# Performance work log

Measured on AMD Instinct MI355X. Metric: run time of the kernel, lower is better.

The kernel has to match this reference:

```python
import jax, jax.numpy as jnp
import numpy as np

EMB = 256
N_NODES = 20000
N_EDGES = 200000


def _sage_layer(x, src, dst, edge_attr, W, b, n_nodes):
    # message = x[src] + edge_attr ; mean-aggregate into dst ; ReLU(Linear([x;agg]))
    msg = x[src] + edge_attr                                   # [2E, emb]
    s = jax.ops.segment_sum(msg, dst, num_segments=n_nodes)    # [N, emb]
    cnt = jax.ops.segment_sum(jnp.ones((dst.shape[0], 1), x.dtype), dst,
                              num_segments=n_nodes)            # [N, 1]
    agg = s / jnp.maximum(cnt, 1.0)
    return jax.nn.relu(jnp.concatenate([x, agg], axis=1) @ W + b)


def setup_inputs() -> dict:
    key = jax.random.key(0)
    ks = jax.random.split(key, 12)
    sc = 0.05
    inp = {
        "x": jax.random.normal(ks[0], (N_NODES, EMB), jnp.float32),
        "edge_attr": jax.random.normal(ks[1], (N_EDGES, EMB), jnp.float32),
        "batch_q_embds": jax.random.normal(ks[2], (N_EDGES, EMB), jnp.float32),
        "edge_index": jax.random.randint(ks[3], (2, N_EDGES), 0, N_NODES, jnp.int64
                                         if jax.config.jax_enable_x64 else jnp.int32),
        "W_rev1": jax.random.normal(ks[4], (EMB, EMB), jnp.float32) * sc,
        "b_rev1": jnp.zeros((EMB,), jnp.float32),
        "W_rev2": jax.random.normal(ks[5], (EMB, EMB), jnp.float32) * sc,
        "b_rev2": jnp.zeros((EMB,), jnp.float32),
        "W_sage1": jax.random.normal(ks[6], (2 * EMB, EMB), jnp.float32) * sc,
        "b_sage1": jnp.zeros((EMB,), jnp.float32),
        "W_sage2": jax.random.normal(ks[7], (2 * EMB, EMB), jnp.float32) * sc,
        "b_sage2": jnp.zeros((EMB,), jnp.float32),
        "W_pred1": jax.random.normal(ks[8], (6 * EMB, EMB), jnp.float32) * sc,
        "b_pred1": jnp.zeros((EMB,), jnp.float32),
        "W_pred2": jax.random.normal(ks[9], (EMB, 1), jnp.float32) * sc,
        "b_pred2": jnp.zeros((1,), jnp.float32),
    }
    return inp


def reference(x, edge_attr, batch_q_embds, edge_index,
              W_rev1, b_rev1, W_rev2, b_rev2,
              W_sage1, b_sage1, W_sage2, b_sage2,
              W_pred1, b_pred1, W_pred2, b_pred2):
    src, dst = edge_index[0], edge_index[1]
    # reverse-edge attributes via proj_reverse MLP
    edge_attr_rev = jax.nn.relu(edge_attr @ W_rev1 + b_rev1) @ W_rev2 + b_rev2
    src_f = jnp.concatenate([src, dst])          # [2E]
    dst_f = jnp.concatenate([dst, src])          # [2E]
    ea_f = jnp.concatenate([edge_attr, edge_attr_rev], axis=0)  # [2E, emb]
    # 2-layer GraphSAGE backbone over nodes, collect per-layer outputs
    h1 = _sage_layer(x, src_f, dst_f, ea_f, W_sage1, b_sage1, N_NODES)
    h2 = _sage_layer(h1, src_f, dst_f, ea_f, W_sage2, b_sage2, N_NODES)
    h_e = jnp.concatenate([h1, h2], axis=1)      # [N, 2*emb]
    # per-edge triple features: [q ; h_e[head] ; edge_attr ; h_e[tail]]
    h_triple = jnp.concatenate([batch_q_embds, h_e[src], edge_attr, h_e[dst]], axis=1)
    attn_logits = (jax.nn.relu(h_triple @ W_pred1 + b_pred1) @ W_pred2 + b_pred2)[:, 0]
    # idp-bern sampling (training=True): gumbel-like logistic noise, temp=1
    u = jax.random.uniform(jax.random.key(42), attn_logits.shape,
                           attn_logits.dtype, 1e-10, 1.0 - 1e-10)
    noise = jnp.log(u) - jnp.log(1.0 - u)
    sampled = jax.nn.sigmoid(attn_logits + noise)
    return attn_logits, sampled
```

## Files before the change

kernel.cpp:

```cpp
#include <hip/hip_runtime.h>
#include <cstdint>
#include <cstddef>

#define EMB 256
#define NN 20000
#define NE 200000
#define NE2 400000

typedef unsigned short ushort_t;
typedef __attribute__((ext_vector_type(8))) short bf16x8;
typedef __attribute__((ext_vector_type(4))) float f32x4;

__device__ __forceinline__ ushort_t f2bf(float f) {
    unsigned u = __float_as_uint(f);
    u += 0x7FFFu + ((u >> 16) & 1u);
    return (ushort_t)(u >> 16);
}
__device__ __forceinline__ float bf2f(ushort_t u) {
    return __uint_as_float(((unsigned)u) << 16);
}

__device__ __forceinline__ void async_cp16(const ushort_t* g, ushort_t* l) {
    __builtin_amdgcn_global_load_lds(
        (const __attribute__((address_space(1))) unsigned int*)g,
        (__attribute__((address_space(3))) unsigned int*)l,
        16, 0, 0);
}

__device__ __forceinline__ unsigned rotl32(unsigned v, int d) {
    return (v << d) | (v >> (32 - d));
}
__device__ __forceinline__ void threefry2x32(unsigned k0, unsigned k1,
                                             unsigned x0, unsigned x1,
                                             unsigned& o0, unsigned& o1) {
    unsigned k2 = k0 ^ k1 ^ 0x1BD11BDAu;
    x0 += k0; x1 += k1;
#define TF_R(r) { x0 += x1; x1 = rotl32(x1, (r)); x1 ^= x0; }
    TF_R(13) TF_R(15) TF_R(26) TF_R(6)
    x0 += k1; x1 += k2 + 1u;
    TF_R(17) TF_R(29) TF_R(16) TF_R(24)
    x0 += k2; x1 += k0 + 2u;
    TF_R(13) TF_R(15) TF_R(26) TF_R(6)
    x0 += k0; x1 += k1 + 3u;
    TF_R(17) TF_R(29) TF_R(16) TF_R(24)
    x0 += k1; x1 += k2 + 4u;
    TF_R(13) TF_R(15) TF_R(26) TF_R(6)
    x0 += k2; x1 += k0 + 5u;
#undef TF_R
    o0 = x0; o1 = x1;
}

__global__ void deg_kernel(const int* __restrict__ src, const int* __restrict__ dst,
                           int* __restrict__ deg) {
    int i = blockIdx.x * blockDim.x + threadIdx.x;
    if (i < NE2) {
        int n = (i < NE) ? dst[i] : src[i - NE];
        atomicAdd(&deg[n], 1);
    }
}

__global__ void prefix_kernel(const int* __restrict__ deg, int* __restrict__ row_start,
                              int* __restrict__ cursor) {
    __shared__ int sums[1024];
    int t = threadIdx.x;
    const int CH = (NN + 1023) / 1024;
    int lo = t * CH, hi = lo + CH;
    if (hi > NN) hi = NN;
    if (lo > NN) lo = NN;
    int s = 0;
    for (int n = lo; n < hi; n++) s += deg[n];
    sums[t] = s;
    __syncthreads();
    for (int off = 1; off < 1024; off <<= 1) {
        int v = (t >= off) ? sums[t - off] : 0;
        __syncthreads();
        sums[t] += v;
        __syncthreads();
    }
    int run = (t == 0) ? 0 : sums[t - 1];
    for (int n = lo; n < hi; n++) {
        row_start[n] = run;
        cursor[n] = run;
        run += deg[n];
    }
    if (t == 1023) row_start[NN] = sums[1023];
}

__global__ void scatter_kernel(const int* __restrict__ src, const int* __restrict__ dst,
                               int* __restrict__ cursor, int* __restrict__ elist) {
    int i = blockIdx.x * blockDim.x + threadIdx.x;
    if (i < NE2) {
        int n = (i < NE) ? dst[i] : src[i - NE];
        int pos = atomicAdd(&cursor[n], 1);
        elist[pos] = i;
    }
}

__global__ void conv_bf_kernel(const float* __restrict__ in, ushort_t* __restrict__ out,
                               int n8) {
    int i = blockIdx.x * 256 + threadIdx.x;
    if (i >= n8) return;
    const float* p = in + (size_t)i * 8;
    float4 a = *(const float4*)p;
    float4 b = *(const float4*)(p + 4);
    union { ushort_t u[8]; uint4 v; } r;
    r.u[0] = f2bf(a.x); r.u[1] = f2bf(a.y); r.u[2] = f2bf(a.z); r.u[3] = f2bf(a.w);
    r.u[4] = f2bf(b.x); r.u[5] = f2bf(b.y); r.u[6] = f2bf(b.z); r.u[7] = f2bf(b.w);
    *(uint4*)(out + (size_t)i * 8) = r.v;
}

__global__ void transpose_bf_kernel(const float* __restrict__ src, ushort_t* __restrict__ dst,
                                    int dstStride, int koff, int Krows) {
    int k = blockIdx.x;
    int n = threadIdx.x;
    dst[(size_t)n * dstStride + koff + k] = f2bf(src[(size_t)k * 256 + n]);
}

template <int KTOT, int EPI>
__global__ __launch_bounds__(256, 2) void mfma_gemm(
        const ushort_t* __restrict__ A0, int rsA0,
        const ushort_t* __restrict__ A1, int rsA1,
        const ushort_t* __restrict__ Bt,
        const float* __restrict__ bias,
        void* __restrict__ out, int rsOut, int M) {
    __shared__ ushort_t As[128 * 32];
    __shared__ ushort_t Bs[256 * 32];

    int tid = threadIdx.x;
    int lane = tid & 63;
    int wave = tid >> 6;
    int wr = wave >> 1;
    int wc = wave & 1;
    int quad = lane >> 4;
    int col_l = lane & 15;
    int bm = blockIdx.x;

    f32x4 acc[4][8];
#pragma unroll
    for (int mt = 0; mt < 4; mt++)
#pragma unroll
        for (int nt = 0; nt < 8; nt++) acc[mt][nt] = (f32x4)0.f;

    for (int k0 = 0; k0 < KTOT; k0 += 32) {
        __syncthreads();
        const ushort_t* abase;
        int rs, koffs;
        if (KTOT == 512 && k0 >= 256) { abase = A1; rs = rsA1; koffs = k0 - 256; }
        else                          { abase = A0; rs = rsA0; koffs = k0; }
#pragma unroll
        for (int j = 0; j < 2; j++) {
            int flat = tid + 256 * j;
            int row = flat >> 2, ch = flat & 3;
            int grow = bm * 128 + row;
            if (grow >= M) grow = M - 1;
            const ushort_t* gp = abase + (size_t)grow * rs + koffs + ch * 8;
            ushort_t* lp = As + ((wave * 64 + 256 * j) * 8);
            async_cp16(gp, lp);
        }
#pragma unroll
        for (int j = 0; j < 4; j++) {
            int flat = tid + 256 * j;
            int n = flat >> 2, ch = flat & 3;
            const ushort_t* gp = Bt + (size_t)n * KTOT + k0 + ch * 8;
            ushort_t* lp = Bs + ((wave * 64 + 256 * j) * 8);
            async_cp16(gp, lp);
        }
        __syncthreads();

        bf16x8 a[4], b[8];
#pragma unroll
        for (int mt = 0; mt < 4; mt++)
            a[mt] = *(const bf16x8*)(As + (wr * 64 + mt * 16 + col_l) * 32 + quad * 8);
#pragma unroll
        for (int nt = 0; nt < 8; nt++)
            b[nt] = *(const bf16x8*)(Bs + (wc * 128 + nt * 16 + col_l) * 32 + quad * 8);
#pragma unroll
        for (int mt = 0; mt < 4; mt++)
#pragma unroll
            for (int nt = 0; nt < 8; nt++)
                acc[mt][nt] = __builtin_amdgcn_mfma_f32_16x16x32_bf16(
                    a[mt], b[nt], acc[mt][nt], 0, 0, 0);
    }

    float bs[8];
    if (EPI >= 2) {
#pragma unroll
        for (int nt = 0; nt < 8; nt++) bs[nt] = bias[wc * 128 + nt * 16 + col_l];
    }
#pragma unroll
    for (int mt = 0; mt < 4; mt++) {
#pragma unroll
        for (int nt = 0; nt < 8; nt++) {
            int colg = wc * 128 + nt * 16 + col_l;
#pragma unroll
            for (int r = 0; r < 4; r++) {
                int rg = bm * 128 + wr * 64 + mt * 16 + quad * 4 + r;
                if (rg < M) {
                    float v = acc[mt][nt][r];
                    if (EPI >= 2) v += bs[nt];
                    if (EPI == 3) v = fmaxf(v, 0.f);
                    if (EPI == 0)
                        ((float*)out)[(size_t)rg * rsOut + colg] = v;
                    else
                        ((ushort_t*)out)[(size_t)rg * rsOut + colg] = f2bf(v);
                }
            }
        }
    }
}

__global__ __launch_bounds__(64) void agg_bf_kernel(
        const ushort_t* __restrict__ xin, int rsx,
        const ushort_t* __restrict__ eaf, const ushort_t* __restrict__ ear,
        const int* __restrict__ src, const int* __restrict__ dst,
        const int* __restrict__ row_start, const int* __restrict__ elist,
        const int* __restrict__ deg, ushort_t* __restrict__ agg) {
    int n = blockIdx.x;
    int c = threadIdx.x * 4;
    float ax = 0.f, ay = 0.f, az = 0.f, aw = 0.f;
    int beg = row_start[n], end = row_start[n + 1];
    for (int p = beg; p < end; p++) {
        int i = elist[p];
        const ushort_t* xr;
        const ushort_t* er;
        if (i < NE) { xr = xin + (size_t)src[i] * rsx; er = eaf + (size_t)i * 256; }
        else { int j = i - NE; xr = xin + (size_t)dst[j] * rsx; er = ear + (size_t)j * 256; }
        ushort4 xv = *(const ushort4*)(xr + c);
        ushort4 ev = *(const ushort4*)(er + c);
        ax += bf2f(xv.x) + bf2f(ev.x);
        ay += bf2f(xv.y) + bf2f(ev.y);
        az += bf2f(xv.z) + bf2f(ev.z);
        aw += bf2f(xv.w) + bf2f(ev.w);
    }
    float d = fmaxf((float)deg[n], 1.0f);
    ushort4 o;
    o.x = f2bf(ax / d); o.y = f2bf(ay / d); o.z = f2bf(az / d); o.w = f2bf(aw / d);
    *(ushort4*)(agg + (size_t)n * 256 + c) = o;
}

__global__ __launch_bounds__(256) void finish_kernel(
        const ushort_t* __restrict__ pre,
        const float* __restrict__ Hs, const float* __restrict__ Hd,
        const int* __restrict__ src, const int* __restrict__ dst,
        const float* __restrict__ b1, const float* __restrict__ w2,
        const float* __restrict__ b2,
        float* __restrict__ out_logits, float* __restrict__ out_sampled) {
    int e = blockIdx.x * 4 + (threadIdx.x >> 6);
    int lane = threadIdx.x & 63;
    int c = lane * 4;
    int s = src[e], d = dst[e];
    ushort4 p4 = *(const ushort4*)(pre + (size_t)e * 256 + c);
    float4 hs = *(const float4*)(Hs + (size_t)s * 256 + c);
    float4 hd = *(const float4*)(Hd + (size_t)d * 256 + c);
    float4 bb = *(const float4*)(b1 + c);
    float4 ww = *(const float4*)(w2 + c);
    float part =
        fmaxf(bf2f(p4.x) + hs.x + hd.x + bb.x, 0.f) * ww.x +
        fmaxf(bf2f(p4.y) + hs.y + hd.y + bb.y, 0.f) * ww.y +
        fmaxf(bf2f(p4.z) + hs.z + hd.z + bb.z, 0.f) * ww.z +
        fmaxf(bf2f(p4.w) + hs.w + hd.w + bb.w, 0.f) * ww.w;
#pragma unroll
    for (int m = 32; m > 0; m >>= 1) part += __shfl_xor(part, m, 64);
    if (lane == 0) {
        float logit = part + b2[0];
        out_logits[e] = logit;
        unsigned y0, y1;
        threefry2x32(0u, 42u, 0u, (unsigned)e, y0, y1);
        unsigned bits = y0 ^ y1;
        float f = __uint_as_float((bits >> 9) | 0x3F800000u) - 1.0f;
        float u = fmaxf(1e-10f, f + 1e-10f);
        float noise = logf(u) - logf(1.0f - u);
        out_sampled[e] = 1.0f / (1.0f + expf(-(logit + noise)));
    }
}

extern "C" void kernel_launch(void* const* d_in, const int* in_sizes, int n_in,
                              void* d_out, int out_size, void* d_ws, size_t ws_size,
                              hipStream_t stream) {
    const float* x        = (const float*)d_in[0];
    const float* ea       = (const float*)d_in[1];
    const float* qemb     = (const float*)d_in[2];
    const int*   eidx     = (const int*)d_in[3];
    const float* W_rev1   = (const float*)d_in[4];
    const float* b_rev1   = (const float*)d_in[5];
    const float* W_rev2   = (const float*)d_in[6];
    const float* b_rev2   = (const float*)d_in[7];
    const float* W_sage1  = (const float*)d_in[8];
    const float* b_sage1  = (const float*)d_in[9];
    const float* W_sage2  = (const float*)d_in[10];
    const float* b_sage2  = (const float*)d_in[11];
    const float* W_pred1  = (const float*)d_in[12];
    const float* b_pred1  = (const float*)d_in[13];
    const float* W_pred2  = (const float*)d_in[14];
    const float* b_pred2  = (const float*)d_in[15];
    float* out = (float*)d_out;

    const int* src = eidx;
    const int* dst = eidx + NE;

    char* w = (char*)d_ws;
    ushort_t* ea_bf  = (ushort_t*)w; w += (size_t)NE * 256 * 2;
    ushort_t* slotA  = (ushort_t*)w; w += (size_t)NE * 256 * 2;
    ushort_t* slotB  = (ushort_t*)w; w += (size_t)NE * 256 * 2;
    ushort_t* x_bf   = (ushort_t*)w; w += (size_t)NN * 256 * 2;
    ushort_t* H      = (ushort_t*)w; w += (size_t)NN * 512 * 2;
    ushort_t* agg_bf = (ushort_t*)w; w += (size_t)NN * 256 * 2;
    float*    Hsrc   = (float*)w;    w += (size_t)NN * 256 * 4;
    float*    Hdst   = (float*)w;    w += (size_t)NN * 256 * 4;
    ushort_t* Wt_rev1  = (ushort_t*)w; w += 256 * 256 * 2;
    ushort_t* Wt_rev2  = (ushort_t*)w; w += 256 * 256 * 2;
    ushort_t* Wt_sage1 = (ushort_t*)w; w += 256 * 512 * 2;
    ushort_t* Wt_sage2 = (ushort_t*)w; w += 256 * 512 * 2;
    ushort_t* Wt_src   = (ushort_t*)w; w += 256 * 512 * 2;
    ushort_t* Wt_dst   = (ushort_t*)w; w += 256 * 512 * 2;
    ushort_t* Wt_edge  = (ushort_t*)w; w += 256 * 512 * 2;
    int* deg       = (int*)w; w += (size_t)NN * 4;
    int* row_start = (int*)w; w += (size_t)(NN + 1) * 4;
    int* cursor    = (int*)w; w += (size_t)NN * 4;
    int* elist     = (int*)w; w += (size_t)NE2 * 4;

    ushort_t* hid_bf    = slotA;
    ushort_t* edge_pre  = slotA;
    ushort_t* ea_rev_bf = slotB;
    ushort_t* q_bf      = slotB;

    const int EB = (NE + 127) / 128;
    const int NB = (NN + 127) / 128;

    hipMemsetAsync(deg, 0, (size_t)NN * 4, stream);
    deg_kernel<<<(NE2 + 255) / 256, 256, 0, stream>>>(src, dst, deg);
    prefix_kernel<<<1, 1024, 0, stream>>>(deg, row_start, cursor);
    scatter_kernel<<<(NE2 + 255) / 256, 256, 0, stream>>>(src, dst, cursor, elist);

    transpose_bf_kernel<<<256, 256, 0, stream>>>(W_rev1, Wt_rev1, 256, 0, 256);
    transpose_bf_kernel<<<256, 256, 0, stream>>>(W_rev2, Wt_rev2, 256, 0, 256);
    transpose_bf_kernel<<<512, 256, 0, stream>>>(W_sage1, Wt_sage1, 512, 0, 512);
    transpose_bf_kernel<<<512, 256, 0, stream>>>(W_sage2, Wt_sage2, 512, 0, 512);
    transpose_bf_kernel<<<512, 256, 0, stream>>>(W_pred1 + (size_t)256 * 256, Wt_src, 512, 0, 512);
    transpose_bf_kernel<<<512, 256, 0, stream>>>(W_pred1 + (size_t)1024 * 256, Wt_dst, 512, 0, 512);
    transpose_bf_kernel<<<256, 256, 0, stream>>>(W_pred1, Wt_edge, 512, 0, 256);
    transpose_bf_kernel<<<256, 256, 0, stream>>>(W_pred1 + (size_t)768 * 256, Wt_edge, 512, 256, 256);

    conv_bf_kernel<<<(NE * 256 / 8 + 255) / 256, 256, 0, stream>>>(ea, ea_bf, NE * 256 / 8);
    conv_bf_kernel<<<(NN * 256 / 8 + 255) / 256, 256, 0, stream>>>(x, x_bf, NN * 256 / 8);

    mfma_gemm<256, 3><<<EB, 256, 0, stream>>>(ea_bf, 256, nullptr, 0, Wt_rev1, b_rev1,
                                              hid_bf, 256, NE);
    mfma_gemm<256, 2><<<EB, 256, 0, stream>>>(hid_bf, 256, nullptr, 0, Wt_rev2, b_rev2,
                                              ea_rev_bf, 256, NE);

    agg_bf_kernel<<<NN, 64, 0, stream>>>(x_bf, 256, ea_bf, ea_rev_bf,
                                         src, dst, row_start, elist, deg, agg_bf);
    mfma_gemm<512, 3><<<NB, 256, 0, stream>>>(x_bf, 256, agg_bf, 256, Wt_sage1, b_sage1,
                                              H, 512, NN);
    agg_bf_kernel<<<NN, 64, 0, stream>>>(H, 512, ea_bf, ea_rev_bf,
                                         src, dst, row_start, elist, deg, agg_bf);
    mfma_gemm<512, 3><<<NB, 256, 0, stream>>>(H, 512, agg_bf, 256, Wt_sage2, b_sage2,
                                              H + 256, 512, NN);

    mfma_gemm<512, 0><<<NB, 256, 0, stream>>>(H, 512, H + 256, 512, Wt_src, nullptr,
                                              Hsrc, 256, NN);
    mfma_gemm<512, 0><<<NB, 256, 0, stream>>>(H, 512, H + 256, 512, Wt_dst, nullptr,
                                              Hdst, 256, NN);

    conv_bf_kernel<<<(NE * 256 / 8 + 255) / 256, 256, 0, stream>>>(qemb, q_bf, NE * 256 / 8);
    mfma_gemm<512, 1><<<EB, 256, 0, stream>>>(q_bf, 256, ea_bf, 256, Wt_edge, nullptr,
                                              edge_pre, 256, NE);

    finish_kernel<<<NE / 4, 256, 0, stream>>>(edge_pre, Hsrc, Hdst, src, dst,
                                              b_pred1, W_pred2, b_pred2,
                                              out, out + NE);
}
```

Baseline: 1.099 ms.

## Fuse edge predictor epilogue into GEMM and batch small conversion launches

The edge GEMM now reads the fp32 query embeddings directly and converts them to bf16 while staging into LDS, which removes a separate conversion pass. Its epilogue also adds the gathered Hsrc/Hdst rows, applies bias, ReLU and the final dot with W_pred2, then writes logits and sampled values, so the bf16 edge_pre round trip and the finish kernel are gone. The eight weight transposes now run as one launch, the two input conversions as one launch, and the src/dst projection GEMMs as one 2D grid. The trade-offs are synchronous loads in place of async LDS copies for the fp32 operand, strided per-row gathers inside the GEMM epilogue, and LDS atomics for the row reduction.

Result: faster. 1.008 ms (-8.2%).

```diff
diff --git a/kernel.cpp b/kernel.cpp
--- a/kernel.cpp
+++ b/kernel.cpp
@@ -96,35 +96,50 @@
     }
 }
 
-__global__ void conv_bf_kernel(const float* __restrict__ in, ushort_t* __restrict__ out,
-                               int n8) {
+__global__ void conv2_kernel(const float* __restrict__ a, ushort_t* __restrict__ oa, int na8,
+                             const float* __restrict__ b, ushort_t* __restrict__ ob, int nb8) {
     int i = blockIdx.x * 256 + threadIdx.x;
-    if (i >= n8) return;
-    const float* p = in + (size_t)i * 8;
-    float4 a = *(const float4*)p;
-    float4 b = *(const float4*)(p + 4);
-    union { ushort_t u[8]; uint4 v; } r;
-    r.u[0] = f2bf(a.x); r.u[1] = f2bf(a.y); r.u[2] = f2bf(a.z); r.u[3] = f2bf(a.w);
-    r.u[4] = f2bf(b.x); r.u[5] = f2bf(b.y); r.u[6] = f2bf(b.z); r.u[7] = f2bf(b.w);
-    *(uint4*)(out + (size_t)i * 8) = r.v;
-}
-
-__global__ void transpose_bf_kernel(const float* __restrict__ src, ushort_t* __restrict__ dst,
-                                    int dstStride, int koff, int Krows) {
+    const float* p;
+    ushort_t* o;
+    if (i < na8) { p = a + (size_t)i * 8; o = oa + (size_t)i * 8; }
+    else {
+        int j = i - na8;
+        if (j >= nb8) return;
+        p = b + (size_t)j * 8; o = ob + (size_t)j * 8;
+    }
+    float4 u = *(const float4*)p;
+    float4 v = *(const float4*)(p + 4);
+    union { ushort_t s[8]; uint4 w; } r;
+    r.s[0] = f2bf(u.x); r.s[1] = f2bf(u.y); r.s[2] = f2bf(u.z); r.s[3] = f2bf(u.w);
+    r.s[4] = f2bf(v.x); r.s[5] = f2bf(v.y); r.s[6] = f2bf(v.z); r.s[7] = f2bf(v.w);
+    *(uint4*)o = r.w;
+}
+
+struct TD { const float* src; ushort_t* dst; int stride, koff, kr; };
+struct TA { TD d[8]; };
+
+__global__ void transpose_all_kernel(TA ta) {
+    TD t = ta.d[blockIdx.y];
     int k = blockIdx.x;
+    if (k >= t.kr) return;
     int n = threadIdx.x;
-    dst[(size_t)n * dstStride + koff + k] = f2bf(src[(size_t)k * 256 + n]);
-}
-
-template <int KTOT, int EPI>
+    t.dst[(size_t)n * t.stride + t.koff + k] = f2bf(t.src[(size_t)k * 256 + n]);
+}
+
+template <int KTOT, int EPI, bool A0F32>
 __global__ __launch_bounds__(256, 2) void mfma_gemm(
-        const ushort_t* __restrict__ A0, int rsA0,
+        const void* __restrict__ A0v, int rsA0,
         const ushort_t* __restrict__ A1, int rsA1,
-        const ushort_t* __restrict__ Bt,
+        const ushort_t* __restrict__ Bt, const ushort_t* __restrict__ Bt2,
         const float* __restrict__ bias,
-        void* __restrict__ out, int rsOut, int M) {
+        void* __restrict__ out, void* __restrict__ out2, int rsOut, int M,
+        const int* __restrict__ srcp, const int* __restrict__ dstp,
+        const float* __restrict__ Hs, const float* __restrict__ Hd,
+        const float* __restrict__ w2, const float* __restrict__ b2v,
+        float* __restrict__ out_s) {
     __shared__ ushort_t As[128 * 32];
     __shared__ ushort_t Bs[256 * 32];
+    __shared__ float red[128];
 
     int tid = threadIdx.x;
     int lane = tid & 63;
@@ -135,6 +150,9 @@
     int col_l = lane & 15;
     int bm = blockIdx.x;
 
+    const ushort_t* Bsel = blockIdx.y ? Bt2 : Bt;
+    void* Osel = blockIdx.y ? out2 : out;
+
     f32x4 acc[4][8];
 #pragma unroll
     for (int mt = 0; mt < 4; mt++)
@@ -143,25 +161,43 @@
 
     for (int k0 = 0; k0 < KTOT; k0 += 32) {
         __syncthreads();
-        const ushort_t* abase;
-        int rs, koffs;
-        if (KTOT == 512 && k0 >= 256) { abase = A1; rs = rsA1; koffs = k0 - 256; }
-        else                          { abase = A0; rs = rsA0; koffs = k0; }
-#pragma unroll
-        for (int j = 0; j < 2; j++) {
-            int flat = tid + 256 * j;
-            int row = flat >> 2, ch = flat & 3;
-            int grow = bm * 128 + row;
-            if (grow >= M) grow = M - 1;
-            const ushort_t* gp = abase + (size_t)grow * rs + koffs + ch * 8;
-            ushort_t* lp = As + ((wave * 64 + 256 * j) * 8);
-            async_cp16(gp, lp);
+        bool seg1 = (KTOT == 512) && (k0 >= 256);
+        if (A0F32 && !seg1) {
+#pragma unroll
+            for (int j = 0; j < 2; j++) {
+                int flat = tid + 256 * j;
+                int row = flat >> 2, ch = flat & 3;
+                int grow = bm * 128 + row;
+                if (grow >= M) grow = M - 1;
+                const float* gp = (const float*)A0v + (size_t)grow * rsA0 + k0 + ch * 8;
+                float4 u = *(const float4*)gp;
+                float4 v = *(const float4*)(gp + 4);
+                union { ushort_t s[8]; uint4 w; } r;
+                r.s[0] = f2bf(u.x); r.s[1] = f2bf(u.y); r.s[2] = f2bf(u.z); r.s[3] = f2bf(u.w);
+                r.s[4] = f2bf(v.x); r.s[5] = f2bf(v.y); r.s[6] = f2bf(v.z); r.s[7] = f2bf(v.w);
+                *(uint4*)(As + (size_t)flat * 8) = r.w;
+            }
+        } else {
+            const ushort_t* abase;
+            int rs, koffs;
+            if (seg1) { abase = A1; rs = rsA1; koffs = k0 - 256; }
+            else      { abase = (const ushort_t*)A0v; rs = rsA0; koffs = k0; }
+#pragma unroll
+            for (int j = 0; j < 2; j++) {
+                int flat = tid + 256 * j;
+                int row = flat >> 2, ch = flat & 3;
+                int grow = bm * 128 + row;
+                if (grow >= M) grow = M - 1;
+                const ushort_t* gp = abase + (size_t)grow * rs + koffs + ch * 8;
+                ushort_t* lp = As + ((wave * 64 + 256 * j) * 8);
+                async_cp16(gp, lp);
+            }
         }
 #pragma unroll
         for (int j = 0; j < 4; j++) {
             int flat = tid + 256 * j;
             int n = flat >> 2, ch = flat & 3;
-            const ushort_t* gp = Bt + (size_t)n * KTOT + k0 + ch * 8;
+            const ushort_t* gp = Bsel + (size_t)n * KTOT + k0 + ch * 8;
             ushort_t* lp = Bs + ((wave * 64 + 256 * j) * 8);
             async_cp16(gp, lp);
         }
@@ -180,6 +216,56 @@
             for (int nt = 0; nt < 8; nt++)
                 acc[mt][nt] = __builtin_amdgcn_mfma_f32_16x16x32_bf16(
                     a[mt], b[nt], acc[mt][nt], 0, 0, 0);
+    }
+
+    if (EPI == 4) {
+        if (tid < 128) red[tid] = 0.f;
+        __syncthreads();
+        float b1c[8], w2c[8];
+#pragma unroll
+        for (int nt = 0; nt < 8; nt++) {
+            int col = wc * 128 + nt * 16 + col_l;
+            b1c[nt] = bias[col];
+            w2c[nt] = w2[col];
+        }
+#pragma unroll
+        for (int mt = 0; mt < 4; mt++) {
+#pragma unroll
+            for (int r = 0; r < 4; r++) {
+                int lrow = wr * 64 + mt * 16 + quad * 4 + r;
+                int e = bm * 128 + lrow;
+                int ec = e < M ? e : M - 1;
+                int s = srcp[ec], d = dstp[ec];
+                const float* hsr = Hs + (size_t)s * 256;
+                const float* hdr = Hd + (size_t)d * 256;
+                float part = 0.f;
+#pragma unroll
+                for (int nt = 0; nt < 8; nt++) {
+                    int col = wc * 128 + nt * 16 + col_l;
+                    part += fmaxf(acc[mt][nt][r] + hsr[col] + hdr[col] + b1c[nt], 0.f)
+                            * w2c[nt];
+                }
+#pragma unroll
+                for (int m = 8; m > 0; m >>= 1) part += __shfl_xor(part, m, 64);
+                if (col_l == 0) atomicAdd(&red[lrow], part);
+            }
+        }
+        __syncthreads();
+        if (tid < 128) {
+            int e = bm * 128 + tid;
+            if (e < M) {
+                float logit = red[tid] + b2v[0];
+                ((float*)out)[e] = logit;
+                unsigned y0, y1;
+                threefry2x32(0u, 42u, 0u, (unsigned)e, y0, y1);
+                unsigned bits = y0 ^ y1;
+                float f = __uint_as_float((bits >> 9) | 0x3F800000u) - 1.0f;
+                float u = fmaxf(1e-10f, f + 1e-10f);
+                float noise = logf(u) - logf(1.0f - u);
+                out_s[e] = 1.0f / (1.0f + expf(-(logit + noise)));
+            }
+        }
+        return;
     }
 
     float bs[8];
@@ -200,9 +286,9 @@
                     if (EPI >= 2) v += bs[nt];
                     if (EPI == 3) v = fmaxf(v, 0.f);
                     if (EPI == 0)
-                        ((float*)out)[(size_t)rg * rsOut + colg] = v;
+                        ((float*)Osel)[(size_t)rg * rsOut + colg] = v;
                     else
-                        ((ushort_t*)out)[(size_t)rg * rsOut + colg] = f2bf(v);
+                        ((ushort_t*)Osel)[(size_t)rg * rsOut + colg] = f2bf(v);
                 }
             }
         }
@@ -238,42 +324,6 @@
     *(ushort4*)(agg + (size_t)n * 256 + c) = o;
 }
 
-__global__ __launch_bounds__(256) void finish_kernel(
-        const ushort_t* __restrict__ pre,
-        const float* __restrict__ Hs, const float* __restrict__ Hd,
-        const int* __restrict__ src, const int* __restrict__ dst,
-        const float* __restrict__ b1, const float* __restrict__ w2,
-        const float* __restrict__ b2,
-        float* __restrict__ out_logits, float* __restrict__ out_sampled) {
-    int e = blockIdx.x * 4 + (threadIdx.x >> 6);
-    int lane = threadIdx.x & 63;
-    int c = lane * 4;
-    int s = src[e], d = dst[e];
-    ushort4 p4 = *(const ushort4*)(pre + (size_t)e * 256 + c);
-    float4 hs = *(const float4*)(Hs + (size_t)s * 256 + c);
-    float4 hd = *(const float4*)(Hd + (size_t)d * 256 + c);
-    float4 bb = *(const float4*)(b1 + c);
-    float4 ww = *(const float4*)(w2 + c);
-    float part =
-        fmaxf(bf2f(p4.x) + hs.x + hd.x + bb.x, 0.f) * ww.x +
-        fmaxf(bf2f(p4.y) + hs.y + hd.y + bb.y, 0.f) * ww.y +
-        fmaxf(bf2f(p4.z) + hs.z + hd.z + bb.z, 0.f) * ww.z +
-        fmaxf(bf2f(p4.w) + hs.w + hd.w + bb.w, 0.f) * ww.w;
-#pragma unroll
-    for (int m = 32; m > 0; m >>= 1) part += __shfl_xor(part, m, 64);
-    if (lane == 0) {
-        float logit = part + b2[0];
-        out_logits[e] = logit;
-        unsigned y0, y1;
-        threefry2x32(0u, 42u, 0u, (unsigned)e, y0, y1);
-        unsigned bits = y0 ^ y1;
-        float f = __uint_as_float((bits >> 9) | 0x3F800000u) - 1.0f;
-        float u = fmaxf(1e-10f, f + 1e-10f);
-        float noise = logf(u) - logf(1.0f - u);
-        out_sampled[e] = 1.0f / (1.0f + expf(-(logit + noise)));
-    }
-}
-
 extern "C" void kernel_launch(void* const* d_in, const int* in_sizes, int n_in,
                               void* d_out, int out_size, void* d_ws, size_t ws_size,
                               hipStream_t stream) {
@@ -300,8 +350,8 @@
 
     char* w = (char*)d_ws;
     ushort_t* ea_bf  = (ushort_t*)w; w += (size_t)NE * 256 * 2;
-    ushort_t* slotA  = (ushort_t*)w; w += (size_t)NE * 256 * 2;
-    ushort_t* slotB  = (ushort_t*)w; w += (size_t)NE * 256 * 2;
+    ushort_t* hid_bf = (ushort_t*)w; w += (size_t)NE * 256 * 2;
+    ushort_t* ea_rev_bf = (ushort_t*)w; w += (size_t)NE * 256 * 2;
     ushort_t* x_bf   = (ushort_t*)w; w += (size_t)NN * 256 * 2;
     ushort_t* H      = (ushort_t*)w; w += (size_t)NN * 512 * 2;
     ushort_t* agg_bf = (ushort_t*)w; w += (size_t)NN * 256 * 2;
@@ -319,11 +369,6 @@
     int* cursor    = (int*)w; w += (size_t)NN * 4;
     int* elist     = (int*)w; w += (size_t)NE2 * 4;
 
-    ushort_t* hid_bf    = slotA;
-    ushort_t* edge_pre  = slotA;
-    ushort_t* ea_rev_bf = slotB;
-    ushort_t* q_bf      = slotB;
-
     const int EB = (NE + 127) / 128;
     const int NB = (NN + 127) / 128;
 
@@ -332,42 +377,44 @@
     prefix_kernel<<<1, 1024, 0, stream>>>(deg, row_start, cursor);
     scatter_kernel<<<(NE2 + 255) / 256, 256, 0, stream>>>(src, dst, cursor, elist);
 
-    transpose_bf_kernel<<<256, 256, 0, stream>>>(W_rev1, Wt_rev1, 256, 0, 256);
-    transpose_bf_kernel<<<256, 256, 0, stream>>>(W_rev2, Wt_rev2, 256, 0, 256);
-    transpose_bf_kernel<<<512, 256, 0, stream>>>(W_sage1, Wt_sage1, 512, 0, 512);
-    transpose_bf_kernel<<<512, 256, 0, stream>>>(W_sage2, Wt_sage2, 512, 0, 512);
-    transpose_bf_kernel<<<512, 256, 0, stream>>>(W_pred1 + (size_t)256 * 256, Wt_src, 512, 0, 512);
-    transpose_bf_kernel<<<512, 256, 0, stream>>>(W_pred1 + (size_t)1024 * 256, Wt_dst, 512, 0, 512);
-    transpose_bf_kernel<<<256, 256, 0, stream>>>(W_pred1, Wt_edge, 512, 0, 256);
-    transpose_bf_kernel<<<256, 256, 0, stream>>>(W_pred1 + (size_t)768 * 256, Wt_edge, 512, 256, 256);
-
-    conv_bf_kernel<<<(NE * 256 / 8 + 255) / 256, 256, 0, stream>>>(ea, ea_bf, NE * 256 / 8);
-    conv_bf_kernel<<<(NN * 256 / 8 + 255) / 256, 256, 0, stream>>>(x, x_bf, NN * 256 / 8);
-
-    mfma_gemm<256, 3><<<EB, 256, 0, stream>>>(ea_bf, 256, nullptr, 0, Wt_rev1, b_rev1,
-                                              hid_bf, 256, NE);
-    mfma_gemm<256, 2><<<EB, 256, 0, stream>>>(hid_bf, 256, nullptr, 0, Wt_rev2, b_rev2,
-                                              ea_rev_bf, 256, NE);
+    TA ta;
+    ta.d[0] = { W_rev1,  Wt_rev1,  256, 0,   256 };
+    ta.d[1] = { W_rev2,  Wt_rev2,  256, 0,   256 };
+    ta.d[2] = { W_sage1, Wt_sage1, 512, 0,   512 };
+    ta.d[3] = { W_sage2, Wt_sage2, 512, 0,   512 };
+    ta.d[4] = { W_pred1 + (size_t)256 * 256,  Wt_src,  512, 0,   512 };
+    ta.d[5] = { W_pred1 + (size_t)1024 * 256, Wt_dst,  512, 0,   512 };
+    ta.d[6] = { W_pred1,                      Wt_edge, 512, 0,   256 };
+    ta.d[7] = { W_pred1 + (size_t)768 * 256,  Wt_edge, 512, 256, 256 };
+    transpose_all_kernel<<<dim3(512, 8), 256, 0, stream>>>(ta);
+
+    conv2_kernel<<<((NE + NN) * 32 + 255) / 256, 256, 0, stream>>>(
+        ea, ea_bf, NE * 32, x, x_bf, NN * 32);
+
+    mfma_gemm<256, 3, false><<<EB, 256, 0, stream>>>(
+        ea_bf, 256, nullptr, 0, Wt_rev1, nullptr, b_rev1,
+        hid_bf, nullptr, 256, NE, nullptr, nullptr, nullptr, nullptr, nullptr, nullptr, nullptr);
+    mfma_gemm<256, 2, false><<<EB, 256, 0, stream>>>(
+        hid_bf, 256, nullptr, 0, Wt_rev2, nullptr, b_rev2,
+        ea_rev_bf, nullptr, 256, NE, nullptr, nullptr, nullptr, nullptr, nullptr, nullptr, nullptr);
 
     agg_bf_kernel<<<NN, 64, 0, stream>>>(x_bf, 256, ea_bf, ea_rev_bf,
                                          src, dst, row_start, elist, deg, agg_bf);
-    mfma_gemm<512, 3><<<NB, 256, 0, stream>>>(x_bf, 256, agg_bf, 256, Wt_sage1, b_sage1,
-                                              H, 512, NN);
+    mfma_gemm<512, 3, false><<<NB, 256, 0, stream>>>(
+        x_bf, 256, agg_bf, 256, Wt_sage1, nullptr, b_sage1,
+        H, nullptr, 512, NN, nullptr, nullptr, nullptr, nullptr, nullptr, nullptr, nullptr);
+
     agg_bf_kernel<<<NN, 64, 0, stream>>>(H, 512, ea_bf, ea_rev_bf,
                                          src, dst, row_start, elist, deg, agg_bf);
-    mfma_gemm<512, 3><<<NB, 256, 0, stream>>>(H, 512, agg_bf, 256, Wt_sage2, b_sage2,
-                                              H + 256, 512, NN);
-
-    mfma_gemm<512, 0><<<NB, 256, 0, stream>>>(H, 512, H + 256, 512, Wt_src, nullptr,
-                                              Hsrc, 256, NN);
-    mfma_gemm<512, 0><<<NB, 256, 0, stream>>>(H, 512, H + 256, 512, Wt_dst, nullptr,
-                                              Hdst, 256, NN);
-
-    conv_bf_kernel<<<(NE * 256 / 8 + 255) / 256, 256, 0, stream>>>(qemb, q_bf, NE * 256 / 8);
-    mfma_gemm<512, 1><<<EB, 256, 0, stream>>>(q_bf, 256, ea_bf, 256, Wt_edge, nullptr,
-                                              edge_pre, 256, NE);
-
-    finish_kernel<<<NE / 4, 256, 0, stream>>>(edge_pre, Hsrc, Hdst, src, dst,
-                                              b_pred1, W_pred2, b_pred2,
-                                              out, out + NE);
-}
+    mfma_gemm<512, 3, false><<<NB, 256, 0, stream>>>(
+        H, 512, agg_bf, 256, Wt_sage2, nullptr, b_sage2,
+        H + 256, nullptr, 512, NN, nullptr, nullptr, nullptr, nullptr, nullptr, nullptr, nullptr);
+
+    mfma_gemm<512, 0, false><<<dim3(NB, 2), 256, 0, stream>>>(
+        H, 512, H + 256, 512, Wt_src, Wt_dst, nullptr,
+        Hsrc, Hdst, 256, NN, nullptr, nullptr, nullptr, nullptr, nullptr, nullptr, nullptr);
+
+    mfma_gemm<512, 4, true><<<EB, 256, 0, stream>>>(
+        qemb, 256, ea_bf, 256, Wt_edge, nullptr, b_pred1,
+        out, nullptr, 0, NE, src, dst, Hsrc, Hdst, W_pred2, b_pred2, out + NE);
+}
```
